# Kernel optimization log

Measured on AMD Instinct MI355X. Metric: run time of the kernel, lower is better.

## Reference

```python
import jax, jax.numpy as jnp
import numpy as np

UNITS = 1024
FEAT = 1024
SEQ = 8192


def setup_inputs() -> dict:
    key = jax.random.key(0)
    ks = jax.random.split(key, 8)
    s = 0.05  # keras RandomUniform(-0.05, 0.05) default-style init
    inputs = jax.random.normal(ks[0], (1, SEQ, FEAT), dtype=jnp.float32)
    f = jax.random.normal(ks[1], (SEQ, 1), dtype=jnp.float32)
    # LSTM params, keras gate order [i, f, c, o]
    W = jax.random.uniform(ks[2], (FEAT, 4 * UNITS), minval=-s, maxval=s, dtype=jnp.float32)
    U = jax.random.uniform(ks[3], (UNITS, 4 * UNITS), minval=-s, maxval=s, dtype=jnp.float32)
    b = jax.random.uniform(ks[4], (4 * UNITS,), minval=-s, maxval=s, dtype=jnp.float32)
    # RackioObserverDense(2, tanh)
    Wd = jax.random.uniform(ks[5], (UNITS, 2), minval=-s, maxval=s, dtype=jnp.float32)
    bd = jax.random.uniform(ks[6], (2,), minval=-s, maxval=s, dtype=jnp.float32)
    return {"inputs": inputs, "f": f, "W": W, "U": U, "b": b, "Wd": Wd, "bd": bd}


def _lstm_linear_act(x, W, U, b):
    # keras LSTM with activation=None: candidate and output activation are identity,
    # recurrent_activation is sigmoid. Gate order i, f, c, o.
    S = x.shape[0]
    units = U.shape[0]
    xz = x @ W + b  # precompute input projection for all steps: (S, 4U)

    def step(carry, xz_t):
        h, c = carry
        z = xz_t + h @ U
        zi, zf, zg, zo = jnp.split(z, 4)
        i = jax.nn.sigmoid(zi)
        fg = jax.nn.sigmoid(zf)
        o = jax.nn.sigmoid(zo)
        c = fg * c + i * zg      # candidate activation = identity
        h = o * c                # output activation = identity
        return (h, c), h

    h0 = jnp.zeros((units,), dtype=x.dtype)
    c0 = jnp.zeros((units,), dtype=x.dtype)
    _, hs = jax.lax.scan(step, (h0, c0), xz)  # (S, units)
    return hs


def reference(inputs, f, W, U, b, Wd, bd):
    x = inputs[0]                               # (S, F); batch must be 1
    hs = _lstm_linear_act(x, W, U, b)           # (S, units), return_sequences=True
    norm = jnp.tanh(hs)                         # self.activation
    h_c = jnp.tanh(norm @ Wd + bd)              # (S, 2), dense with tanh
    # Vectorized finite-difference write into H (original: nested scalar .assign loop)
    # H[i, j] = (h_c[0, i] - h_c[1, i]) / (f[1, j] - f[2, j])
    num = (h_c[0, :] - h_c[1, :])[:, None]      # (2, 1)
    den = (f[1, :] - f[2, :])[None, :]          # (1, 1)
    H = num / den                               # (2, 1)
    h_out = h_c[0, :].reshape(2, 1)
    return (h_out, H)
```

## Files before the change

kernel.cpp:

```cpp
#include <hip/hip_runtime.h>
#include <math.h>

#define UNITS 1024
#define FEAT  1024
#define GATES 4096

#define OFF_Z0  0
#define OFF_Z1X (GATES)
#define OFF_Z1  (2*GATES)

__device__ __forceinline__ float sigmoidf(float x) { return 1.0f / (1.0f + expf(-x)); }

__device__ __forceinline__ int col_group(int bx) {
    return ((bx & 7) << 5) + (bx >> 3);
}

__global__ __launch_bounds__(256) void k_xw(const float* __restrict__ x,
                                            const float* __restrict__ W,
                                            const float* __restrict__ b,
                                            float* __restrict__ ws) {
    int tid = threadIdx.x;
    int c0 = col_group(blockIdx.x) * 16;

    __shared__ float xs0[FEAT], xs1[FEAT];
    {
        float4 v0 = *reinterpret_cast<const float4*>(&x[tid * 4]);
        float4 v1 = *reinterpret_cast<const float4*>(&x[FEAT + tid * 4]);
        *reinterpret_cast<float4*>(&xs0[tid * 4]) = v0;
        *reinterpret_cast<float4*>(&xs1[tid * 4]) = v1;
    }
    __syncthreads();

    int q = tid & 3;
    int rowbase = tid >> 2;
    const float* wp = W + (size_t)rowbase * GATES + c0 + q * 4;
    float4 a0 = make_float4(0.f, 0.f, 0.f, 0.f);
    float4 a1 = make_float4(0.f, 0.f, 0.f, 0.f);
#pragma unroll
    for (int it = 0; it < 16; ++it) {
        int row = it * 64 + rowbase;
        float4 w = *reinterpret_cast<const float4*>(wp + (size_t)it * 64 * GATES);
        float x0 = xs0[row], x1 = xs1[row];
        a0.x += x0 * w.x; a0.y += x0 * w.y; a0.z += x0 * w.z; a0.w += x0 * w.w;
        a1.x += x1 * w.x; a1.y += x1 * w.y; a1.z += x1 * w.z; a1.w += x1 * w.w;
    }
#pragma unroll
    for (int s = 32; s >= 4; s >>= 1) {
        a0.x += __shfl_down(a0.x, s); a0.y += __shfl_down(a0.y, s);
        a0.z += __shfl_down(a0.z, s); a0.w += __shfl_down(a0.w, s);
        a1.x += __shfl_down(a1.x, s); a1.y += __shfl_down(a1.y, s);
        a1.z += __shfl_down(a1.z, s); a1.w += __shfl_down(a1.w, s);
    }
    __shared__ float4 p0[4][4], p1[4][4];
    int wave = tid >> 6, lane = tid & 63;
    if (lane < 4) { p0[wave][lane] = a0; p1[wave][lane] = a1; }
    __syncthreads();
    if (tid < 4) {
        float4 s0 = p0[0][tid], s1 = p1[0][tid];
#pragma unroll
        for (int w = 1; w < 4; ++w) {
            s0.x += p0[w][tid].x; s0.y += p0[w][tid].y; s0.z += p0[w][tid].z; s0.w += p0[w][tid].w;
            s1.x += p1[w][tid].x; s1.y += p1[w][tid].y; s1.z += p1[w][tid].z; s1.w += p1[w][tid].w;
        }
        float4 bb = *reinterpret_cast<const float4*>(&b[c0 + tid * 4]);
        s0.x += bb.x; s0.y += bb.y; s0.z += bb.z; s0.w += bb.w;
        s1.x += bb.x; s1.y += bb.y; s1.z += bb.z; s1.w += bb.w;
        *reinterpret_cast<float4*>(&ws[OFF_Z0 + c0 + tid * 4]) = s0;
        *reinterpret_cast<float4*>(&ws[OFF_Z1X + c0 + tid * 4]) = s1;
    }
}

__global__ __launch_bounds__(256) void k_hu(const float* __restrict__ U,
                                            float* __restrict__ ws) {
    int tid = threadIdx.x;
    int c0 = col_group(blockIdx.x) * 16;

    __shared__ float h0s[UNITS];
    {
        int u0 = tid * 4;
        float4 zi = *reinterpret_cast<const float4*>(&ws[OFF_Z0 + u0]);
        float4 zg = *reinterpret_cast<const float4*>(&ws[OFF_Z0 + 2 * UNITS + u0]);
        float4 zo = *reinterpret_cast<const float4*>(&ws[OFF_Z0 + 3 * UNITS + u0]);
        float4 h;
        h.x = sigmoidf(zo.x) * (sigmoidf(zi.x) * zg.x);
        h.y = sigmoidf(zo.y) * (sigmoidf(zi.y) * zg.y);
        h.z = sigmoidf(zo.z) * (sigmoidf(zi.z) * zg.z);
        h.w = sigmoidf(zo.w) * (sigmoidf(zi.w) * zg.w);
        *reinterpret_cast<float4*>(&h0s[u0]) = h;
    }
    __syncthreads();

    int q = tid & 3;
    int rowbase = tid >> 2;
    const float* up = U + (size_t)rowbase * GATES + c0 + q * 4;
    float4 a = make_float4(0.f, 0.f, 0.f, 0.f);
#pragma unroll
    for (int it = 0; it < 16; ++it) {
        int row = it * 64 + rowbase;
        float4 u4 = *reinterpret_cast<const float4*>(up + (size_t)it * 64 * GATES);
        float h = h0s[row];
        a.x += h * u4.x; a.y += h * u4.y; a.z += h * u4.z; a.w += h * u4.w;
    }
#pragma unroll
    for (int s = 32; s >= 4; s >>= 1) {
        a.x += __shfl_down(a.x, s); a.y += __shfl_down(a.y, s);
        a.z += __shfl_down(a.z, s); a.w += __shfl_down(a.w, s);
    }
    __shared__ float4 pu[4][4];
    int wave = tid >> 6, lane = tid & 63;
    if (lane < 4) pu[wave][lane] = a;
    __syncthreads();
    if (tid < 4) {
        float4 s = pu[0][tid];
#pragma unroll
        for (int w = 1; w < 4; ++w) {
            s.x += pu[w][tid].x; s.y += pu[w][tid].y; s.z += pu[w][tid].z; s.w += pu[w][tid].w;
        }
        float4 zx = *reinterpret_cast<const float4*>(&ws[OFF_Z1X + c0 + tid * 4]);
        s.x += zx.x; s.y += zx.y; s.z += zx.z; s.w += zx.w;
        *reinterpret_cast<float4*>(&ws[OFF_Z1 + c0 + tid * 4]) = s;
    }
}

__global__ __launch_bounds__(1024) void k_final(const float* __restrict__ ws,
                                                const float* __restrict__ f,
                                                const float* __restrict__ Wd,
                                                const float* __restrict__ bd,
                                                float* __restrict__ out) {
    int u = threadIdx.x;
    const float* Z0 = ws + OFF_Z0;
    const float* Z1 = ws + OFF_Z1;
    float c0 = sigmoidf(Z0[u]) * Z0[u + 2 * UNITS];
    float h0 = sigmoidf(Z0[u + 3 * UNITS]) * c0;
    float c1 = sigmoidf(Z1[u + UNITS]) * c0 + sigmoidf(Z1[u]) * Z1[u + 2 * UNITS];
    float h1 = sigmoidf(Z1[u + 3 * UNITS]) * c1;

    float n0 = tanhf(h0);
    float n1 = tanhf(h1);
    float2 wd = *reinterpret_cast<const float2*>(&Wd[2 * u]);

    float4 v = make_float4(n0 * wd.x, n0 * wd.y, n1 * wd.x, n1 * wd.y);
#pragma unroll
    for (int s = 32; s > 0; s >>= 1) {
        v.x += __shfl_down(v.x, s);
        v.y += __shfl_down(v.y, s);
        v.z += __shfl_down(v.z, s);
        v.w += __shfl_down(v.w, s);
    }
    __shared__ float4 wred[16];
    int wave = u >> 6;
    if ((u & 63) == 0) wred[wave] = v;
    __syncthreads();
    if (u == 0) {
        float4 sa = wred[0];
#pragma unroll
        for (int w = 1; w < 16; ++w) {
            float4 t = wred[w];
            sa.x += t.x; sa.y += t.y; sa.z += t.z; sa.w += t.w;
        }
        float hc00 = tanhf(sa.x + bd[0]);
        float hc01 = tanhf(sa.y + bd[1]);
        float hc10 = tanhf(sa.z + bd[0]);
        float hc11 = tanhf(sa.w + bd[1]);
        float den = f[1] - f[2];
        out[0] = hc00;
        out[1] = hc01;
        out[2] = (hc00 - hc10) / den;
        out[3] = (hc01 - hc11) / den;
    }
}

extern "C" void kernel_launch(void* const* d_in, const int* in_sizes, int n_in,
                              void* d_out, int out_size, void* d_ws, size_t ws_size,
                              hipStream_t stream) {
    const float* x  = (const float*)d_in[0];
    const float* f  = (const float*)d_in[1];
    const float* W  = (const float*)d_in[2];
    const float* U  = (const float*)d_in[3];
    const float* b  = (const float*)d_in[4];
    const float* Wd = (const float*)d_in[5];
    const float* bd = (const float*)d_in[6];
    float* out = (float*)d_out;
    float* ws  = (float*)d_ws;

    k_xw   <<<256, 256, 0, stream>>>(x, W, b, ws);
    k_hu   <<<256, 256, 0, stream>>>(U, ws);
    k_final<<<  1, 1024, 0, stream>>>(ws, f, Wd, bd, out);
}
```

Measured before the change: 105.8 us.

## Fuse LSTM steps into one cooperative kernel with grid sync and prefetched U

Replaces the three-kernel sequence with a single cooperative launch that computes the input projection, does a grid-wide sync, then the recurrent matvec, with a last-block-done atomic counter handling the dense/tanh epilogue. Each thread loads its U slice into registers before the W pass so the U traffic overlaps the first phase. This removes two kernel launch gaps and the separate final kernel. In exchange it adds grid-sync overhead and higher register pressure from holding 16 float4 values per thread. It falls back to the old kernels if the cooperative launch fails.

```diff
diff --git a/kernel.cpp b/kernel.cpp
--- a/kernel.cpp
+++ b/kernel.cpp
@@ -1,18 +1,220 @@
 #include <hip/hip_runtime.h>
+#include <hip/hip_cooperative_groups.h>
 #include <math.h>
 
 #define UNITS 1024
 #define FEAT  1024
 #define GATES 4096
 
+#define FOFF_Z0   0
+#define FOFF_Z1   GATES
+#define FOFF_FLAG (2 * GATES)
+
 #define OFF_Z0  0
 #define OFF_Z1X (GATES)
-#define OFF_Z1  (2*GATES)
+#define OFF_Z1L (2 * GATES)
 
 __device__ __forceinline__ float sigmoidf(float x) { return 1.0f / (1.0f + expf(-x)); }
 
 __device__ __forceinline__ int col_group(int bx) {
     return ((bx & 7) << 5) + (bx >> 3);
+}
+
+__global__ __launch_bounds__(256, 1) void k_fused(
+        const float* __restrict__ x,
+        const float* __restrict__ W,
+        const float* __restrict__ U,
+        const float* __restrict__ b,
+        const float* __restrict__ f,
+        const float* __restrict__ Wd,
+        const float* __restrict__ bd,
+        float* __restrict__ ws,
+        float* __restrict__ out) {
+    int tid = threadIdx.x;
+    int c0 = col_group(blockIdx.x) * 16;
+
+    __shared__ float xs0[FEAT], xs1[FEAT];
+    __shared__ float h0s[UNITS], c0s[UNITS];
+    __shared__ float z1xs[16];
+    __shared__ float4 pr0[4][4], pr1[4][4];
+    __shared__ float4 wred[4];
+    __shared__ int lastflag;
+
+    if (blockIdx.x == 0 && tid == 0) {
+        __hip_atomic_store((int*)&ws[FOFF_FLAG], 0, __ATOMIC_RELAXED,
+                           __HIP_MEMORY_SCOPE_AGENT);
+    }
+
+    {
+        float4 v0 = *reinterpret_cast<const float4*>(&x[tid * 4]);
+        float4 v1 = *reinterpret_cast<const float4*>(&x[FEAT + tid * 4]);
+        *reinterpret_cast<float4*>(&xs0[tid * 4]) = v0;
+        *reinterpret_cast<float4*>(&xs1[tid * 4]) = v1;
+    }
+    __syncthreads();
+
+    int q = tid & 3;
+    int rowbase = tid >> 2;
+    const float* wp = W + (size_t)rowbase * GATES + c0 + q * 4;
+    const float* up = U + (size_t)rowbase * GATES + c0 + q * 4;
+
+    float4 ureg[16];
+#pragma unroll
+    for (int it = 0; it < 16; ++it)
+        ureg[it] = *reinterpret_cast<const float4*>(up + (size_t)it * 64 * GATES);
+
+    float4 a0 = make_float4(0.f, 0.f, 0.f, 0.f);
+    float4 a1 = make_float4(0.f, 0.f, 0.f, 0.f);
+#pragma unroll
+    for (int it = 0; it < 16; ++it) {
+        int row = it * 64 + rowbase;
+        float4 wv = *reinterpret_cast<const float4*>(wp + (size_t)it * 64 * GATES);
+        float x0v = xs0[row], x1v = xs1[row];
+        a0.x += x0v * wv.x; a0.y += x0v * wv.y; a0.z += x0v * wv.z; a0.w += x0v * wv.w;
+        a1.x += x1v * wv.x; a1.y += x1v * wv.y; a1.z += x1v * wv.z; a1.w += x1v * wv.w;
+    }
+#pragma unroll
+    for (int s = 32; s >= 4; s >>= 1) {
+        a0.x += __shfl_down(a0.x, s); a0.y += __shfl_down(a0.y, s);
+        a0.z += __shfl_down(a0.z, s); a0.w += __shfl_down(a0.w, s);
+        a1.x += __shfl_down(a1.x, s); a1.y += __shfl_down(a1.y, s);
+        a1.z += __shfl_down(a1.z, s); a1.w += __shfl_down(a1.w, s);
+    }
+    int wave = tid >> 6, lane = tid & 63;
+    if (lane < 4) { pr0[wave][lane] = a0; pr1[wave][lane] = a1; }
+    __syncthreads();
+    if (tid < 4) {
+        float4 s0 = pr0[0][tid], s1 = pr1[0][tid];
+#pragma unroll
+        for (int w = 1; w < 4; ++w) {
+            s0.x += pr0[w][tid].x; s0.y += pr0[w][tid].y;
+            s0.z += pr0[w][tid].z; s0.w += pr0[w][tid].w;
+            s1.x += pr1[w][tid].x; s1.y += pr1[w][tid].y;
+            s1.z += pr1[w][tid].z; s1.w += pr1[w][tid].w;
+        }
+        float4 bb = *reinterpret_cast<const float4*>(&b[c0 + tid * 4]);
+        s0.x += bb.x; s0.y += bb.y; s0.z += bb.z; s0.w += bb.w;
+        s1.x += bb.x; s1.y += bb.y; s1.z += bb.z; s1.w += bb.w;
+        *reinterpret_cast<float4*>(&ws[FOFF_Z0 + c0 + tid * 4]) = s0;
+        *reinterpret_cast<float4*>(&z1xs[tid * 4]) = s1;
+        __threadfence();
+    }
+
+    cooperative_groups::this_grid().sync();
+
+    {
+        int u0 = tid * 4;
+        float4 zi = *reinterpret_cast<const float4*>(&ws[FOFF_Z0 + u0]);
+        float4 zg = *reinterpret_cast<const float4*>(&ws[FOFF_Z0 + 2 * UNITS + u0]);
+        float4 zo = *reinterpret_cast<const float4*>(&ws[FOFF_Z0 + 3 * UNITS + u0]);
+        float4 cc, hh;
+        cc.x = sigmoidf(zi.x) * zg.x;  hh.x = sigmoidf(zo.x) * cc.x;
+        cc.y = sigmoidf(zi.y) * zg.y;  hh.y = sigmoidf(zo.y) * cc.y;
+        cc.z = sigmoidf(zi.z) * zg.z;  hh.z = sigmoidf(zo.z) * cc.z;
+        cc.w = sigmoidf(zi.w) * zg.w;  hh.w = sigmoidf(zo.w) * cc.w;
+        *reinterpret_cast<float4*>(&c0s[u0]) = cc;
+        *reinterpret_cast<float4*>(&h0s[u0]) = hh;
+    }
+    __syncthreads();
+
+    float4 a = make_float4(0.f, 0.f, 0.f, 0.f);
+#pragma unroll
+    for (int it = 0; it < 16; ++it) {
+        float h = h0s[it * 64 + rowbase];
+        a.x += h * ureg[it].x; a.y += h * ureg[it].y;
+        a.z += h * ureg[it].z; a.w += h * ureg[it].w;
+    }
+#pragma unroll
+    for (int s = 32; s >= 4; s >>= 1) {
+        a.x += __shfl_down(a.x, s); a.y += __shfl_down(a.y, s);
+        a.z += __shfl_down(a.z, s); a.w += __shfl_down(a.w, s);
+    }
+    if (lane < 4) pr0[wave][lane] = a;
+    __syncthreads();
+    if (tid < 4) {
+        float4 s = pr0[0][tid];
+#pragma unroll
+        for (int w = 1; w < 4; ++w) {
+            s.x += pr0[w][tid].x; s.y += pr0[w][tid].y;
+            s.z += pr0[w][tid].z; s.w += pr0[w][tid].w;
+        }
+        float4 zx = *reinterpret_cast<const float4*>(&z1xs[tid * 4]);
+        s.x += zx.x; s.y += zx.y; s.z += zx.z; s.w += zx.w;
+        *reinterpret_cast<float4*>(&ws[FOFF_Z1 + c0 + tid * 4]) = s;
+        __threadfence();
+    }
+    __syncthreads();
+
+    if (tid == 0) {
+        int prev = __hip_atomic_fetch_add((int*)&ws[FOFF_FLAG], 1,
+                                          __ATOMIC_ACQ_REL, __HIP_MEMORY_SCOPE_AGENT);
+        lastflag = (prev == (int)gridDim.x - 1) ? 1 : 0;
+    }
+    __syncthreads();
+    if (!lastflag) return;
+    __threadfence();
+
+    {
+        int u0 = tid * 4;
+        const float* Z1 = ws + FOFF_Z1;
+        float4 zi1 = *reinterpret_cast<const float4*>(&Z1[u0]);
+        float4 zf1 = *reinterpret_cast<const float4*>(&Z1[UNITS + u0]);
+        float4 zg1 = *reinterpret_cast<const float4*>(&Z1[2 * UNITS + u0]);
+        float4 zo1 = *reinterpret_cast<const float4*>(&Z1[3 * UNITS + u0]);
+        float4 cc = *reinterpret_cast<const float4*>(&c0s[u0]);
+        float4 hh = *reinterpret_cast<const float4*>(&h0s[u0]);
+        float4 wdA = *reinterpret_cast<const float4*>(&Wd[2 * u0]);
+        float4 wdB = *reinterpret_cast<const float4*>(&Wd[2 * u0 + 4]);
+        float4 v = make_float4(0.f, 0.f, 0.f, 0.f);
+        float c1, h1, n0, n1;
+
+        c1 = sigmoidf(zf1.x) * cc.x + sigmoidf(zi1.x) * zg1.x;
+        h1 = sigmoidf(zo1.x) * c1;
+        n0 = tanhf(hh.x); n1 = tanhf(h1);
+        v.x += n0 * wdA.x; v.y += n0 * wdA.y; v.z += n1 * wdA.x; v.w += n1 * wdA.y;
+
+        c1 = sigmoidf(zf1.y) * cc.y + sigmoidf(zi1.y) * zg1.y;
+        h1 = sigmoidf(zo1.y) * c1;
+        n0 = tanhf(hh.y); n1 = tanhf(h1);
+        v.x += n0 * wdA.z; v.y += n0 * wdA.w; v.z += n1 * wdA.z; v.w += n1 * wdA.w;
+
+        c1 = sigmoidf(zf1.z) * cc.z + sigmoidf(zi1.z) * zg1.z;
+        h1 = sigmoidf(zo1.z) * c1;
+        n0 = tanhf(hh.z); n1 = tanhf(h1);
+        v.x += n0 * wdB.x; v.y += n0 * wdB.y; v.z += n1 * wdB.x; v.w += n1 * wdB.y;
+
+        c1 = sigmoidf(zf1.w) * cc.w + sigmoidf(zi1.w) * zg1.w;
+        h1 = sigmoidf(zo1.w) * c1;
+        n0 = tanhf(hh.w); n1 = tanhf(h1);
+        v.x += n0 * wdB.z; v.y += n0 * wdB.w; v.z += n1 * wdB.z; v.w += n1 * wdB.w;
+
+#pragma unroll
+        for (int s = 32; s > 0; s >>= 1) {
+            v.x += __shfl_down(v.x, s);
+            v.y += __shfl_down(v.y, s);
+            v.z += __shfl_down(v.z, s);
+            v.w += __shfl_down(v.w, s);
+        }
+        if ((tid & 63) == 0) wred[tid >> 6] = v;
+        __syncthreads();
+        if (tid == 0) {
+            float4 sa = wred[0];
+#pragma unroll
+            for (int w = 1; w < 4; ++w) {
+                float4 t = wred[w];
+                sa.x += t.x; sa.y += t.y; sa.z += t.z; sa.w += t.w;
+            }
+            float hc00 = tanhf(sa.x + bd[0]);
+            float hc01 = tanhf(sa.y + bd[1]);
+            float hc10 = tanhf(sa.z + bd[0]);
+            float hc11 = tanhf(sa.w + bd[1]);
+            float den = f[1] - f[2];
+            out[0] = hc00;
+            out[1] = hc01;
+            out[2] = (hc00 - hc10) / den;
+            out[3] = (hc01 - hc11) / den;
+        }
+    }
 }
 
 __global__ __launch_bounds__(256) void k_xw(const float* __restrict__ x,
@@ -39,10 +241,10 @@
 #pragma unroll
     for (int it = 0; it < 16; ++it) {
         int row = it * 64 + rowbase;
-        float4 w = *reinterpret_cast<const float4*>(wp + (size_t)it * 64 * GATES);
+        float4 wv = *reinterpret_cast<const float4*>(wp + (size_t)it * 64 * GATES);
         float x0 = xs0[row], x1 = xs1[row];
-        a0.x += x0 * w.x; a0.y += x0 * w.y; a0.z += x0 * w.z; a0.w += x0 * w.w;
-        a1.x += x1 * w.x; a1.y += x1 * w.y; a1.z += x1 * w.z; a1.w += x1 * w.w;
+        a0.x += x0 * wv.x; a0.y += x0 * wv.y; a0.z += x0 * wv.z; a0.w += x0 * wv.w;
+        a1.x += x1 * wv.x; a1.y += x1 * wv.y; a1.z += x1 * wv.z; a1.w += x1 * wv.w;
     }
 #pragma unroll
     for (int s = 32; s >= 4; s >>= 1) {
@@ -118,7 +320,7 @@
         }
         float4 zx = *reinterpret_cast<const float4*>(&ws[OFF_Z1X + c0 + tid * 4]);
         s.x += zx.x; s.y += zx.y; s.z += zx.z; s.w += zx.w;
-        *reinterpret_cast<float4*>(&ws[OFF_Z1 + c0 + tid * 4]) = s;
+        *reinterpret_cast<float4*>(&ws[OFF_Z1L + c0 + tid * 4]) = s;
     }
 }
 
@@ -129,7 +331,7 @@
                                                 float* __restrict__ out) {
     int u = threadIdx.x;
     const float* Z0 = ws + OFF_Z0;
-    const float* Z1 = ws + OFF_Z1;
+    const float* Z1 = ws + OFF_Z1L;
     float c0 = sigmoidf(Z0[u]) * Z0[u + 2 * UNITS];
     float h0 = sigmoidf(Z0[u + 3 * UNITS]) * c0;
     float c1 = sigmoidf(Z1[u + UNITS]) * c0 + sigmoidf(Z1[u]) * Z1[u + 2 * UNITS];
@@ -183,7 +385,14 @@
     float* out = (float*)d_out;
     float* ws  = (float*)d_ws;
 
-    k_xw   <<<256, 256, 0, stream>>>(x, W, b, ws);
-    k_hu   <<<256, 256, 0, stream>>>(U, ws);
-    k_final<<<  1, 1024, 0, stream>>>(ws, f, Wd, bd, out);
-}
+    void* args[] = {(void*)&x, (void*)&W, (void*)&U, (void*)&b,
+                    (void*)&f, (void*)&Wd, (void*)&bd, (void*)&ws, (void*)&out};
+    hipError_t err = hipLaunchCooperativeKernel(
+        reinterpret_cast<const void*>(&k_fused), dim3(256), dim3(256), args, 0, stream);
+    if (err != hipSuccess) {
+        (void)hipGetLastError();
+        k_xw   <<<256, 256, 0, stream>>>(x, W, b, ws);
+        k_hu   <<<256, 256, 0, stream>>>(U, ws);
+        k_final<<<  1, 1024, 0, stream>>>(ws, f, Wd, bd, out);
+    }
+}
```

After: 173.9 us. 64.4% more time.

## Fuse LSTM stages into one kernel with atomic flags and U prefetch

Applied to the files above, without the earlier changes.

Merges the three launches into a single 512-block kernel. The first 256 blocks compute the input projection and bump a global counter. The other 256 blocks preload their U tiles into registers, spin until the counter is complete, then do the recurrent matvec, and the last block to finish runs the dense/tanh epilogue. The aim is to remove launch gaps and overlap the U load with the W stage. The risks are spin-wait deadlock if the U blocks occupy the GPU before the W blocks are scheduled, and heavy register use for the prefetch.

```diff
diff --git a/kernel.cpp b/kernel.cpp
--- a/kernel.cpp
+++ b/kernel.cpp
@@ -9,164 +9,223 @@
 #define OFF_Z1X (GATES)
 #define OFF_Z1  (2*GATES)
 
+__device__ int g_w_done = 0;
+__device__ int g_u_done = 0;
+
 __device__ __forceinline__ float sigmoidf(float x) { return 1.0f / (1.0f + expf(-x)); }
 
 __device__ __forceinline__ int col_group(int bx) {
     return ((bx & 7) << 5) + (bx >> 3);
 }
 
-__global__ __launch_bounds__(256) void k_xw(const float* __restrict__ x,
-                                            const float* __restrict__ W,
-                                            const float* __restrict__ b,
-                                            float* __restrict__ ws) {
+__global__ __launch_bounds__(256, 2) void k_lstm(
+        const float* __restrict__ x,
+        const float* __restrict__ W,
+        const float* __restrict__ U,
+        const float* __restrict__ b,
+        const float* __restrict__ f,
+        const float* __restrict__ Wd,
+        const float* __restrict__ bd,
+        float* __restrict__ ws,
+        float* __restrict__ out) {
     int tid = threadIdx.x;
-    int c0 = col_group(blockIdx.x) * 16;
-
-    __shared__ float xs0[FEAT], xs1[FEAT];
-    {
-        float4 v0 = *reinterpret_cast<const float4*>(&x[tid * 4]);
-        float4 v1 = *reinterpret_cast<const float4*>(&x[FEAT + tid * 4]);
-        *reinterpret_cast<float4*>(&xs0[tid * 4]) = v0;
-        *reinterpret_cast<float4*>(&xs1[tid * 4]) = v1;
-    }
-    __syncthreads();
-
-    int q = tid & 3;
-    int rowbase = tid >> 2;
-    const float* wp = W + (size_t)rowbase * GATES + c0 + q * 4;
-    float4 a0 = make_float4(0.f, 0.f, 0.f, 0.f);
-    float4 a1 = make_float4(0.f, 0.f, 0.f, 0.f);
-#pragma unroll
-    for (int it = 0; it < 16; ++it) {
-        int row = it * 64 + rowbase;
-        float4 w = *reinterpret_cast<const float4*>(wp + (size_t)it * 64 * GATES);
-        float x0 = xs0[row], x1 = xs1[row];
-        a0.x += x0 * w.x; a0.y += x0 * w.y; a0.z += x0 * w.z; a0.w += x0 * w.w;
-        a1.x += x1 * w.x; a1.y += x1 * w.y; a1.z += x1 * w.z; a1.w += x1 * w.w;
-    }
-#pragma unroll
-    for (int s = 32; s >= 4; s >>= 1) {
-        a0.x += __shfl_down(a0.x, s); a0.y += __shfl_down(a0.y, s);
-        a0.z += __shfl_down(a0.z, s); a0.w += __shfl_down(a0.w, s);
-        a1.x += __shfl_down(a1.x, s); a1.y += __shfl_down(a1.y, s);
-        a1.z += __shfl_down(a1.z, s); a1.w += __shfl_down(a1.w, s);
-    }
-    __shared__ float4 p0[4][4], p1[4][4];
     int wave = tid >> 6, lane = tid & 63;
-    if (lane < 4) { p0[wave][lane] = a0; p1[wave][lane] = a1; }
-    __syncthreads();
-    if (tid < 4) {
-        float4 s0 = p0[0][tid], s1 = p1[0][tid];
-#pragma unroll
-        for (int w = 1; w < 4; ++w) {
-            s0.x += p0[w][tid].x; s0.y += p0[w][tid].y; s0.z += p0[w][tid].z; s0.w += p0[w][tid].w;
-            s1.x += p1[w][tid].x; s1.y += p1[w][tid].y; s1.z += p1[w][tid].z; s1.w += p1[w][tid].w;
-        }
-        float4 bb = *reinterpret_cast<const float4*>(&b[c0 + tid * 4]);
-        s0.x += bb.x; s0.y += bb.y; s0.z += bb.z; s0.w += bb.w;
-        s1.x += bb.x; s1.y += bb.y; s1.z += bb.z; s1.w += bb.w;
-        *reinterpret_cast<float4*>(&ws[OFF_Z0 + c0 + tid * 4]) = s0;
-        *reinterpret_cast<float4*>(&ws[OFF_Z1X + c0 + tid * 4]) = s1;
-    }
-}
-
-__global__ __launch_bounds__(256) void k_hu(const float* __restrict__ U,
-                                            float* __restrict__ ws) {
-    int tid = threadIdx.x;
-    int c0 = col_group(blockIdx.x) * 16;
-
-    __shared__ float h0s[UNITS];
+    int q = tid & 3, rowbase = tid >> 2;
+
+    __shared__ float sm[2048];
+    __shared__ float4 pr0[4][4], pr1[4][4];
+    __shared__ float4 wred[4];
+    __shared__ int lastflag;
+
+    if (blockIdx.x < 256) {
+        int c0 = col_group(blockIdx.x) * 16;
+        {
+            float4 v0 = *reinterpret_cast<const float4*>(&x[tid * 4]);
+            float4 v1 = *reinterpret_cast<const float4*>(&x[FEAT + tid * 4]);
+            *reinterpret_cast<float4*>(&sm[tid * 4]) = v0;
+            *reinterpret_cast<float4*>(&sm[FEAT + tid * 4]) = v1;
+        }
+        __syncthreads();
+
+        const float* wp = W + (size_t)rowbase * GATES + c0 + q * 4;
+        float4 a0 = make_float4(0.f, 0.f, 0.f, 0.f);
+        float4 a1 = make_float4(0.f, 0.f, 0.f, 0.f);
+#pragma unroll
+        for (int it = 0; it < 16; ++it) {
+            int row = it * 64 + rowbase;
+            float4 wv = *reinterpret_cast<const float4*>(wp + (size_t)it * 64 * GATES);
+            float x0 = sm[row], x1 = sm[FEAT + row];
+            a0.x += x0 * wv.x; a0.y += x0 * wv.y; a0.z += x0 * wv.z; a0.w += x0 * wv.w;
+            a1.x += x1 * wv.x; a1.y += x1 * wv.y; a1.z += x1 * wv.z; a1.w += x1 * wv.w;
+        }
+#pragma unroll
+        for (int s = 32; s >= 4; s >>= 1) {
+            a0.x += __shfl_down(a0.x, s); a0.y += __shfl_down(a0.y, s);
+            a0.z += __shfl_down(a0.z, s); a0.w += __shfl_down(a0.w, s);
+            a1.x += __shfl_down(a1.x, s); a1.y += __shfl_down(a1.y, s);
+            a1.z += __shfl_down(a1.z, s); a1.w += __shfl_down(a1.w, s);
+        }
+        if (lane < 4) { pr0[wave][lane] = a0; pr1[wave][lane] = a1; }
+        __syncthreads();
+        if (tid < 4) {
+            float4 s0 = pr0[0][tid], s1 = pr1[0][tid];
+#pragma unroll
+            for (int w = 1; w < 4; ++w) {
+                s0.x += pr0[w][tid].x; s0.y += pr0[w][tid].y;
+                s0.z += pr0[w][tid].z; s0.w += pr0[w][tid].w;
+                s1.x += pr1[w][tid].x; s1.y += pr1[w][tid].y;
+                s1.z += pr1[w][tid].z; s1.w += pr1[w][tid].w;
+            }
+            float4 bb = *reinterpret_cast<const float4*>(&b[c0 + tid * 4]);
+            s0.x += bb.x; s0.y += bb.y; s0.z += bb.z; s0.w += bb.w;
+            s1.x += bb.x; s1.y += bb.y; s1.z += bb.z; s1.w += bb.w;
+            *reinterpret_cast<float4*>(&ws[OFF_Z0 + c0 + tid * 4]) = s0;
+            *reinterpret_cast<float4*>(&ws[OFF_Z1X + c0 + tid * 4]) = s1;
+        }
+        __syncthreads();
+        if (tid == 0) {
+            __hip_atomic_fetch_add(&g_w_done, 1, __ATOMIC_RELEASE,
+                                   __HIP_MEMORY_SCOPE_AGENT);
+        }
+        return;
+    }
+
+    int c0 = col_group(blockIdx.x - 256) * 16;
+    const float* up = U + (size_t)rowbase * GATES + c0 + q * 4;
+
+    float4 ureg[16];
+#pragma unroll
+    for (int it = 0; it < 16; ++it)
+        ureg[it] = *reinterpret_cast<const float4*>(up + (size_t)it * 64 * GATES);
+#pragma unroll
+    for (int it = 0; it < 16; ++it)
+        asm volatile("" : "+v"(ureg[it].x), "+v"(ureg[it].y),
+                          "+v"(ureg[it].z), "+v"(ureg[it].w));
+
+    if (tid == 0) {
+        while (__hip_atomic_load(&g_w_done, __ATOMIC_RELAXED,
+                                 __HIP_MEMORY_SCOPE_AGENT) < 256)
+            __builtin_amdgcn_s_sleep(2);
+        (void)__hip_atomic_load(&g_w_done, __ATOMIC_ACQUIRE,
+                                __HIP_MEMORY_SCOPE_AGENT);
+    }
+    __syncthreads();
+
     {
         int u0 = tid * 4;
         float4 zi = *reinterpret_cast<const float4*>(&ws[OFF_Z0 + u0]);
         float4 zg = *reinterpret_cast<const float4*>(&ws[OFF_Z0 + 2 * UNITS + u0]);
         float4 zo = *reinterpret_cast<const float4*>(&ws[OFF_Z0 + 3 * UNITS + u0]);
-        float4 h;
-        h.x = sigmoidf(zo.x) * (sigmoidf(zi.x) * zg.x);
-        h.y = sigmoidf(zo.y) * (sigmoidf(zi.y) * zg.y);
-        h.z = sigmoidf(zo.z) * (sigmoidf(zi.z) * zg.z);
-        h.w = sigmoidf(zo.w) * (sigmoidf(zi.w) * zg.w);
-        *reinterpret_cast<float4*>(&h0s[u0]) = h;
-    }
-    __syncthreads();
-
-    int q = tid & 3;
-    int rowbase = tid >> 2;
-    const float* up = U + (size_t)rowbase * GATES + c0 + q * 4;
+        float4 cc, hh;
+        cc.x = sigmoidf(zi.x) * zg.x;  hh.x = sigmoidf(zo.x) * cc.x;
+        cc.y = sigmoidf(zi.y) * zg.y;  hh.y = sigmoidf(zo.y) * cc.y;
+        cc.z = sigmoidf(zi.z) * zg.z;  hh.z = sigmoidf(zo.z) * cc.z;
+        cc.w = sigmoidf(zi.w) * zg.w;  hh.w = sigmoidf(zo.w) * cc.w;
+        *reinterpret_cast<float4*>(&sm[u0]) = hh;
+        *reinterpret_cast<float4*>(&sm[UNITS + u0]) = cc;
+    }
+    __syncthreads();
+
     float4 a = make_float4(0.f, 0.f, 0.f, 0.f);
 #pragma unroll
     for (int it = 0; it < 16; ++it) {
-        int row = it * 64 + rowbase;
-        float4 u4 = *reinterpret_cast<const float4*>(up + (size_t)it * 64 * GATES);
-        float h = h0s[row];
-        a.x += h * u4.x; a.y += h * u4.y; a.z += h * u4.z; a.w += h * u4.w;
+        float h = sm[it * 64 + rowbase];
+        a.x += h * ureg[it].x; a.y += h * ureg[it].y;
+        a.z += h * ureg[it].z; a.w += h * ureg[it].w;
     }
 #pragma unroll
     for (int s = 32; s >= 4; s >>= 1) {
         a.x += __shfl_down(a.x, s); a.y += __shfl_down(a.y, s);
         a.z += __shfl_down(a.z, s); a.w += __shfl_down(a.w, s);
     }
-    __shared__ float4 pu[4][4];
-    int wave = tid >> 6, lane = tid & 63;
-    if (lane < 4) pu[wave][lane] = a;
+    if (lane < 4) pr0[wave][lane] = a;
     __syncthreads();
     if (tid < 4) {
-        float4 s = pu[0][tid];
+        float4 s = pr0[0][tid];
 #pragma unroll
         for (int w = 1; w < 4; ++w) {
-            s.x += pu[w][tid].x; s.y += pu[w][tid].y; s.z += pu[w][tid].z; s.w += pu[w][tid].w;
+            s.x += pr0[w][tid].x; s.y += pr0[w][tid].y;
+            s.z += pr0[w][tid].z; s.w += pr0[w][tid].w;
         }
         float4 zx = *reinterpret_cast<const float4*>(&ws[OFF_Z1X + c0 + tid * 4]);
         s.x += zx.x; s.y += zx.y; s.z += zx.z; s.w += zx.w;
         *reinterpret_cast<float4*>(&ws[OFF_Z1 + c0 + tid * 4]) = s;
     }
-}
-
-__global__ __launch_bounds__(1024) void k_final(const float* __restrict__ ws,
-                                                const float* __restrict__ f,
-                                                const float* __restrict__ Wd,
-                                                const float* __restrict__ bd,
-                                                float* __restrict__ out) {
-    int u = threadIdx.x;
-    const float* Z0 = ws + OFF_Z0;
-    const float* Z1 = ws + OFF_Z1;
-    float c0 = sigmoidf(Z0[u]) * Z0[u + 2 * UNITS];
-    float h0 = sigmoidf(Z0[u + 3 * UNITS]) * c0;
-    float c1 = sigmoidf(Z1[u + UNITS]) * c0 + sigmoidf(Z1[u]) * Z1[u + 2 * UNITS];
-    float h1 = sigmoidf(Z1[u + 3 * UNITS]) * c1;
-
-    float n0 = tanhf(h0);
-    float n1 = tanhf(h1);
-    float2 wd = *reinterpret_cast<const float2*>(&Wd[2 * u]);
-
-    float4 v = make_float4(n0 * wd.x, n0 * wd.y, n1 * wd.x, n1 * wd.y);
-#pragma unroll
-    for (int s = 32; s > 0; s >>= 1) {
-        v.x += __shfl_down(v.x, s);
-        v.y += __shfl_down(v.y, s);
-        v.z += __shfl_down(v.z, s);
-        v.w += __shfl_down(v.w, s);
-    }
-    __shared__ float4 wred[16];
-    int wave = u >> 6;
-    if ((u & 63) == 0) wred[wave] = v;
-    __syncthreads();
-    if (u == 0) {
-        float4 sa = wred[0];
-#pragma unroll
-        for (int w = 1; w < 16; ++w) {
-            float4 t = wred[w];
-            sa.x += t.x; sa.y += t.y; sa.z += t.z; sa.w += t.w;
-        }
-        float hc00 = tanhf(sa.x + bd[0]);
-        float hc01 = tanhf(sa.y + bd[1]);
-        float hc10 = tanhf(sa.z + bd[0]);
-        float hc11 = tanhf(sa.w + bd[1]);
-        float den = f[1] - f[2];
-        out[0] = hc00;
-        out[1] = hc01;
-        out[2] = (hc00 - hc10) / den;
-        out[3] = (hc01 - hc11) / den;
+    __syncthreads();
+
+    if (tid == 0) {
+        int prev = __hip_atomic_fetch_add(&g_u_done, 1, __ATOMIC_ACQ_REL,
+                                          __HIP_MEMORY_SCOPE_AGENT);
+        lastflag = (prev == 255) ? 1 : 0;
+    }
+    __syncthreads();
+    if (!lastflag) return;
+
+    {
+        int u0 = tid * 4;
+        const float* Z1 = ws + OFF_Z1;
+        float4 zi1 = *reinterpret_cast<const float4*>(&Z1[u0]);
+        float4 zf1 = *reinterpret_cast<const float4*>(&Z1[UNITS + u0]);
+        float4 zg1 = *reinterpret_cast<const float4*>(&Z1[2 * UNITS + u0]);
+        float4 zo1 = *reinterpret_cast<const float4*>(&Z1[3 * UNITS + u0]);
+        float4 hh = *reinterpret_cast<const float4*>(&sm[u0]);
+        float4 cc = *reinterpret_cast<const float4*>(&sm[UNITS + u0]);
+        float4 wdA = *reinterpret_cast<const float4*>(&Wd[2 * u0]);
+        float4 wdB = *reinterpret_cast<const float4*>(&Wd[2 * u0 + 4]);
+        float4 v = make_float4(0.f, 0.f, 0.f, 0.f);
+        float c1, h1, n0, n1;
+
+        c1 = sigmoidf(zf1.x) * cc.x + sigmoidf(zi1.x) * zg1.x;
+        h1 = sigmoidf(zo1.x) * c1;
+        n0 = tanhf(hh.x); n1 = tanhf(h1);
+        v.x += n0 * wdA.x; v.y += n0 * wdA.y; v.z += n1 * wdA.x; v.w += n1 * wdA.y;
+
+        c1 = sigmoidf(zf1.y) * cc.y + sigmoidf(zi1.y) * zg1.y;
+        h1 = sigmoidf(zo1.y) * c1;
+        n0 = tanhf(hh.y); n1 = tanhf(h1);
+        v.x += n0 * wdA.z; v.y += n0 * wdA.w; v.z += n1 * wdA.z; v.w += n1 * wdA.w;
+
+        c1 = sigmoidf(zf1.z) * cc.z + sigmoidf(zi1.z) * zg1.z;
+        h1 = sigmoidf(zo1.z) * c1;
+        n0 = tanhf(hh.z); n1 = tanhf(h1);
+        v.x += n0 * wdB.x; v.y += n0 * wdB.y; v.z += n1 * wdB.x; v.w += n1 * wdB.y;
+
+        c1 = sigmoidf(zf1.w) * cc.w + sigmoidf(zi1.w) * zg1.w;
+        h1 = sigmoidf(zo1.w) * c1;
+        n0 = tanhf(hh.w); n1 = tanhf(h1);
+        v.x += n0 * wdB.z; v.y += n0 * wdB.w; v.z += n1 * wdB.z; v.w += n1 * wdB.w;
+
+#pragma unroll
+        for (int s = 32; s > 0; s >>= 1) {
+            v.x += __shfl_down(v.x, s);
+            v.y += __shfl_down(v.y, s);
+            v.z += __shfl_down(v.z, s);
+            v.w += __shfl_down(v.w, s);
+        }
+        if ((tid & 63) == 0) wred[tid >> 6] = v;
+        __syncthreads();
+        if (tid == 0) {
+            float4 sa = wred[0];
+#pragma unroll
+            for (int w = 1; w < 4; ++w) {
+                float4 t = wred[w];
+                sa.x += t.x; sa.y += t.y; sa.z += t.z; sa.w += t.w;
+            }
+            float hc00 = tanhf(sa.x + bd[0]);
+            float hc01 = tanhf(sa.y + bd[1]);
+            float hc10 = tanhf(sa.z + bd[0]);
+            float hc11 = tanhf(sa.w + bd[1]);
+            float den = f[1] - f[2];
+            out[0] = hc00;
+            out[1] = hc01;
+            out[2] = (hc00 - hc10) / den;
+            out[3] = (hc01 - hc11) / den;
+
+            __hip_atomic_store(&g_w_done, 0, __ATOMIC_RELAXED,
+                               __HIP_MEMORY_SCOPE_AGENT);
+            __hip_atomic_store(&g_u_done, 0, __ATOMIC_RELAXED,
+                               __HIP_MEMORY_SCOPE_AGENT);
+        }
     }
 }
 
@@ -183,7 +242,5 @@
     float* out = (float*)d_out;
     float* ws  = (float*)d_ws;
 
-    k_xw   <<<256, 256, 0, stream>>>(x, W, b, ws);
-    k_hu   <<<256, 256, 0, stream>>>(U, ws);
-    k_final<<<  1, 1024, 0, stream>>>(ws, f, Wd, bd, out);
+    k_lstm<<<512, 256, 0, stream>>>(x, W, U, b, f, Wd, bd, ws, out);
 }
```

Measured after the change: 128.6 us. 1.22x slower.
